# Optimization experiments

Measured on AMD Instinct MI355X. Metric: run time of the kernel, lower is better.

Reference implementation:

```python
import jax, jax.numpy as jnp
import numpy as np

N_NODES = 50000
N_EDGES = 600000
HIDDEN = 128
N_GRAPHS = 64


def _lin_params(key, din, dout):
    kw, kb = jax.random.split(key)
    W = jax.random.normal(kw, (din, dout), jnp.float32) / np.sqrt(din).astype(np.float32)
    b = jax.random.normal(kb, (dout,), jnp.float32) * 0.01
    return W, b


def setup_inputs() -> dict:
    key = jax.random.key(0)
    ks = jax.random.split(key, 12)
    node_weight = jax.random.uniform(ks[0], (N_NODES,), jnp.float32)
    edge_weight = jax.random.uniform(ks[1], (N_EDGES,), jnp.float32)
    edge_index = jax.random.randint(ks[2], (2, N_EDGES), 0, N_NODES, dtype=jnp.int64)
    batch = jnp.sort(jax.random.randint(ks[3], (N_NODES,), 0, N_GRAPHS, dtype=jnp.int64))
    Wn, bn = _lin_params(ks[4], 1, HIDDEN)
    We, be = _lin_params(ks[5], 1, HIDDEN)
    W1a, b1a = _lin_params(ks[6], HIDDEN, HIDDEN)
    W1b, b1b = _lin_params(ks[7], HIDDEN, HIDDEN)
    W2a, b2a = _lin_params(ks[8], HIDDEN, HIDDEN)
    W2b, b2b = _lin_params(ks[9], HIDDEN, HIDDEN)
    Wm1, bm1 = _lin_params(ks[10], HIDDEN, HIDDEN)
    Wm2, bm2 = _lin_params(ks[11], HIDDEN, 1)
    return dict(node_weight=node_weight, edge_weight=edge_weight, edge_index=edge_index,
                batch=batch, Wn=Wn, bn=bn, We=We, be=be,
                W1a=W1a, b1a=b1a, W1b=W1b, b1b=b1b,
                W2a=W2a, b2a=b2a, W2b=W2b, b2b=b2b,
                Wm1=Wm1, bm1=bm1, Wm2=Wm2, bm2=bm2)


def _gine(x, src, dst, edge_attr, Wa, ba, Wb, bb):
    # GINEConv (eps=0): h_i = nn( x_i + sum_{j->i} ReLU(x_j + e_ji) )
    msg = jax.nn.relu(x[src] + edge_attr)              # [E, H]
    agg = jax.ops.segment_sum(msg, dst, num_segments=N_NODES)  # [N, H]
    h = x + agg
    h = jax.nn.leaky_relu(h @ Wa + ba, 0.01)
    return h @ Wb + bb


def reference(node_weight, edge_weight, edge_index, batch,
              Wn, bn, We, be, W1a, b1a, W1b, b1b,
              W2a, b2a, W2b, b2b, Wm1, bm1, Wm2, bm2):
    src, dst = edge_index[0], edge_index[1]
    x = node_weight[:, None] @ Wn + bn                 # [N, H]
    e = edge_weight[:, None] @ We + be                 # [E, H]
    x = jax.nn.relu(_gine(x, src, dst, e, W1a, b1a, W1b, b1b))
    x = jax.nn.relu(_gine(x, src, dst, e, W2a, b2a, W2b, b2b))
    # global mean pool over graphs
    sums = jax.ops.segment_sum(x, batch, num_segments=N_GRAPHS)        # [G, H]
    cnts = jax.ops.segment_sum(jnp.ones((N_NODES,), x.dtype), batch, num_segments=N_GRAPHS)
    pooled = sums / jnp.maximum(cnts, 1.0)[:, None]
    h = jax.nn.leaky_relu(pooled @ Wm1 + bm1, 0.01)
    out = jax.nn.sigmoid(h @ Wm2 + bm2)                # [G, 1]
    return out[:, 0]
```

## Files before the change

### kernel.cpp

```cpp
#include <hip/hip_runtime.h>
#include <math.h>

#define NN 50000
#define NE 600000
#define HID 128
#define NG 64
#define CAP 48
#define ASTRH 136
#define NBIN 196
#define CHUNK 2344
#define TR 64

using half8v = __attribute__((ext_vector_type(8))) _Float16;
using half4v = __attribute__((ext_vector_type(4))) _Float16;
using half2v = __attribute__((ext_vector_type(2))) _Float16;
using f32x4  = __attribute__((ext_vector_type(4))) float;

__device__ __forceinline__ float unpack_w(unsigned p) {
  return (float)__builtin_bit_cast(_Float16, (unsigned short)(p & 0xffffu));
}

__global__ void k_prep(const int* __restrict__ batch, float* __restrict__ gsum,
                       int* __restrict__ pos,
                       const float* __restrict__ W1a, const float* __restrict__ W1b,
                       const float* __restrict__ W2a, const float* __restrict__ W2b,
                       _Float16* __restrict__ whi,
                       const int* __restrict__ dst, int* __restrict__ hist) {
  __shared__ int lh[NBIN];
  int b = blockIdx.x, t = threadIdx.x;
  if (b < 196) {
    int i = b * 256 + t;
    if (i < NN) {
      int bb = batch[i];
      if (i == 0) {
        for (int g = 0; g <= bb; ++g) pos[g] = 0;
      } else {
        int bp = batch[i - 1];
        for (int g = bp + 1; g <= bb; ++g) pos[g] = i;
      }
      if (i == NN - 1) {
        for (int g = bb + 1; g <= NG; ++g) pos[g] = NN;
      }
    }
  } else if (b < 204) {
    int i = (b - 196) * 256 + t;
    if (i < 2048) reinterpret_cast<float4*>(gsum)[i] = make_float4(0.f, 0.f, 0.f, 0.f);
  } else if (b < 236) {
    int tid = (b - 204) * 256 + t;
    int m = tid >> 11;
    const float* W = (m == 0) ? W1a : (m == 1) ? W1b : (m == 2) ? W2a : W2b;
    int rem = tid & 2047;
    int kt = rem >> 9;
    int fj = (rem >> 6) & 7;
    int l = rem & 63;
    int col = fj * 16 + (l & 15);
    int kbase = kt * 32 + (l >> 4) * 8;
    size_t obase = (size_t)m * 16384 + (size_t)(((kt * 8 + fj) * 64 + l)) * 8;
#pragma unroll
    for (int j = 0; j < 8; ++j) {
      whi[obase + j] = (_Float16)W[(size_t)(kbase + j) * HID + col];
    }
  } else {
    int hb = b - 236;
    if (t < NBIN) lh[t] = 0;
    __syncthreads();
    int lo = hb * CHUNK, hi = min(lo + CHUNK, NE);
    for (int e = lo + t; e < hi; e += 256) atomicAdd(&lh[dst[e] >> 8], 1);
    __syncthreads();
    if (t < NBIN) hist[t * 256 + hb] = lh[t];
  }
}

__global__ void k_scatter(const int* __restrict__ src, const int* __restrict__ dst,
                          const float* __restrict__ ew, const int* __restrict__ hist,
                          int* __restrict__ gbinbase, int2* __restrict__ part) {
  __shared__ int ps[256];
  __shared__ int cur[NBIN];
  int b = blockIdx.x, t = threadIdx.x;
  int sum0 = 0, T = 0;
  if (t < NBIN) {
    const int* row = &hist[t * 256];
#pragma unroll 4
    for (int i = 0; i < 256; ++i) {
      int v = row[i];
      T += v;
      sum0 += (i < b) ? v : 0;
    }
  }
  ps[t] = T;
  __syncthreads();
  for (int d = 1; d < 256; d <<= 1) {
    int u = (t >= d) ? ps[t - d] : 0;
    __syncthreads();
    ps[t] += u;
    __syncthreads();
  }
  if (t < NBIN) {
    int ebase = ps[t] - T;
    cur[t] = ebase + sum0;
    if (b == 0) gbinbase[t] = ebase;
  }
  if (b == 0 && t == 0) gbinbase[NBIN] = NE;
  __syncthreads();
  int lo = b * CHUNK, hi = min(lo + CHUNK, NE);
  for (int e = lo + t; e < hi; e += 256) {
    int d0 = dst[e];
    int p = atomicAdd(&cur[d0 >> 8], 1);
    _Float16 w = (_Float16)ew[e];
    unsigned wb = (unsigned)__builtin_bit_cast(unsigned short, w);
    part[p] = make_int2(src[e], ((d0 & 255) << 16) | (int)wb);
  }
}

__global__ void k_binfill(const int2* __restrict__ part, const int* __restrict__ gbinbase,
                          unsigned* __restrict__ bkt, int* __restrict__ deg) {
  __shared__ int cur[256];
  int j = blockIdx.x, t = threadIdx.x;
  cur[t] = 0;
  __syncthreads();
  int lo = gbinbase[j], hi = gbinbase[j + 1];
  for (int e = lo + t; e < hi; e += 256) {
    int2 q = part[e];
    int dl = q.y >> 16;
    int p = atomicAdd(&cur[dl], 1);
    if (p < CAP)
      bkt[(size_t)((j << 8) + dl) * CAP + p] =
          ((unsigned)q.x << 16) | ((unsigned)q.y & 0xffffu);
  }
  __syncthreads();
  int node = (j << 8) + t;
  if (node < NN) deg[node] = cur[t];
}

__global__ void k_layer1(const float* __restrict__ nw, const unsigned* __restrict__ bkt,
                         const int* __restrict__ deg,
                         const float* __restrict__ Wn, const float* __restrict__ bn,
                         const float* __restrict__ We, const float* __restrict__ be,
                         _Float16* __restrict__ h) {
  int wave = threadIdx.x >> 6;
  int lane = threadIdx.x & 63;
  int node = blockIdx.x * 4 + wave;
  if (node >= NN) return;
  int c = lane * 2;
  float wn0 = Wn[c], wn1 = Wn[c + 1];
  float we0 = We[c], we1 = We[c + 1];
  float bn0 = bn[c], bn1 = bn[c + 1];
  float cb0 = bn0 + be[c], cb1 = bn1 + be[c + 1];
  float ai = nw[node];
  float acc0 = fmaf(ai, wn0, bn0);
  float acc1 = fmaf(ai, wn1, bn1);
  int k0 = node * CAP;
  int cnt = min(deg[node], CAP);
  int k = 0;
  for (; k + 4 <= cnt; k += 4) {
    uint4 q = *reinterpret_cast<const uint4*>(&bkt[k0 + k]);
    float a0 = nw[q.x >> 16], a1 = nw[q.y >> 16];
    float a2 = nw[q.z >> 16], a3 = nw[q.w >> 16];
    float e0 = unpack_w(q.x), e1 = unpack_w(q.y);
    float e2 = unpack_w(q.z), e3 = unpack_w(q.w);
    acc0 += fmaxf(fmaf(a0, wn0, fmaf(e0, we0, cb0)), 0.f);
    acc1 += fmaxf(fmaf(a0, wn1, fmaf(e0, we1, cb1)), 0.f);
    acc0 += fmaxf(fmaf(a1, wn0, fmaf(e1, we0, cb0)), 0.f);
    acc1 += fmaxf(fmaf(a1, wn1, fmaf(e1, we1, cb1)), 0.f);
    acc0 += fmaxf(fmaf(a2, wn0, fmaf(e2, we0, cb0)), 0.f);
    acc1 += fmaxf(fmaf(a2, wn1, fmaf(e2, we1, cb1)), 0.f);
    acc0 += fmaxf(fmaf(a3, wn0, fmaf(e3, we0, cb0)), 0.f);
    acc1 += fmaxf(fmaf(a3, wn1, fmaf(e3, we1, cb1)), 0.f);
  }
  for (; k < cnt; ++k) {
    unsigned p = bkt[k0 + k];
    float a = nw[p >> 16];
    float b = unpack_w(p);
    acc0 += fmaxf(fmaf(a, wn0, fmaf(b, we0, cb0)), 0.f);
    acc1 += fmaxf(fmaf(a, wn1, fmaf(b, we1, cb1)), 0.f);
  }
  half2v o; o[0] = (_Float16)acc0; o[1] = (_Float16)acc1;
  *reinterpret_cast<half2v*>(&h[(size_t)node * HID + c]) = o;
}

__global__ void k_layer2(const _Float16* __restrict__ x1, const unsigned* __restrict__ bkt,
                         const int* __restrict__ deg,
                         const float* __restrict__ We, const float* __restrict__ be,
                         _Float16* __restrict__ h) {
  int wave = threadIdx.x >> 6;
  int l = threadIdx.x & 63;
  int half = l >> 5;
  int lane32 = l & 31;
  int node = blockIdx.x * 8 + wave * 2 + half;
  int c = lane32 * 4;
  float4 w4 = *reinterpret_cast<const float4*>(&We[c]);
  float4 b4 = *reinterpret_cast<const float4*>(&be[c]);
  half4v xs = *reinterpret_cast<const half4v*>(&x1[(size_t)node * HID + c]);
  float acc0 = (float)xs[0], acc1 = (float)xs[1];
  float acc2 = (float)xs[2], acc3 = (float)xs[3];
  int cnt = min(deg[node], CAP);
  int cntO = __shfl_xor(cnt, 32);
  int kmax = max(cnt, cntO);
  int k0 = node * CAP;

  for (int k = 0; k < kmax; k += 8) {
    uint4 qa = *reinterpret_cast<const uint4*>(&bkt[k0 + k]);
    uint4 qb = *reinterpret_cast<const uint4*>(&bkt[k0 + k + 4]);
    unsigned qs[8] = {qa.x, qa.y, qa.z, qa.w, qb.x, qb.y, qb.z, qb.w};
    half4v r[8];
#pragma unroll
    for (int i = 0; i < 8; ++i) {
      int s = min((int)(qs[i] >> 16), NN - 1);
      r[i] = *reinterpret_cast<const half4v*>(&x1[(size_t)s * HID + c]);
    }
#pragma unroll
    for (int i = 0; i < 8; ++i) {
      bool v = (k + i) < cnt;
      float e = unpack_w(qs[i]);
      float m0 = fmaxf((float)r[i][0] + fmaf(e, w4.x, b4.x), 0.f);
      float m1 = fmaxf((float)r[i][1] + fmaf(e, w4.y, b4.y), 0.f);
      float m2 = fmaxf((float)r[i][2] + fmaf(e, w4.z, b4.z), 0.f);
      float m3 = fmaxf((float)r[i][3] + fmaf(e, w4.w, b4.w), 0.f);
      acc0 += v ? m0 : 0.f;
      acc1 += v ? m1 : 0.f;
      acc2 += v ? m2 : 0.f;
      acc3 += v ? m3 : 0.f;
    }
  }
  half4v o;
  o[0] = (_Float16)acc0; o[1] = (_Float16)acc1;
  o[2] = (_Float16)acc2; o[3] = (_Float16)acc3;
  *reinterpret_cast<half4v*>(&h[(size_t)node * HID + c]) = o;
}

template <int POOL>
__global__ __launch_bounds__(256, 6) void k_mlp(
    const _Float16* __restrict__ X,
    const _Float16* __restrict__ Wah, const float* __restrict__ ba,
    const _Float16* __restrict__ Wbh, const float* __restrict__ bb,
    _Float16* __restrict__ Y,
    const int* __restrict__ batch, float* __restrict__ gsum) {
  extern __shared__ char smem_raw[];
  _Float16* Ah = (_Float16*)smem_raw;
  int* sB = (int*)(smem_raw + TR * ASTRH * 2);
  const int tid = threadIdx.x;
  const int l = tid & 63;
  const int wrow = (tid >> 6) * 16;
  const int rowBase = blockIdx.x * TR;

  if (POOL && tid < TR) sB[tid] = batch[min(rowBase + tid, NN - 1)];

  {
    int rr = tid >> 4;
    int c0 = (tid & 15) * 8;
#pragma unroll
    for (int p = 0; p < 4; ++p) {
      int r = p * 16 + rr;
      int srcRow = min(rowBase + r, NN - 1);
      half8v v = *reinterpret_cast<const half8v*>(&X[(size_t)srcRow * HID + c0]);
      *reinterpret_cast<half8v*>(&Ah[r * ASTRH + c0]) = v;
    }
  }
  __syncthreads();

  const int arow0 = wrow + (l & 15);
  const int kgrp = (l >> 4) * 8;
  const int lcol = l & 15;

  f32x4 acc[8];
#pragma unroll
  for (int j = 0; j < 8; ++j) acc[j] = f32x4{0.f, 0.f, 0.f, 0.f};

#pragma unroll
  for (int ks = 0; ks < 4; ++ks) {
    half8v a0 = *reinterpret_cast<const half8v*>(&Ah[arow0 * ASTRH + ks * 32 + kgrp]);
    const _Float16* wbh = &Wah[(size_t)((ks * 8) * 64 + l) * 8];
#pragma unroll
    for (int fj = 0; fj < 8; ++fj) {
      half8v bh = *reinterpret_cast<const half8v*>(wbh + fj * 512);
      acc[fj] = __builtin_amdgcn_mfma_f32_16x16x32_f16(a0, bh, acc[fj], 0, 0, 0);
    }
  }

  {
    float bal[8];
#pragma unroll
    for (int fj = 0; fj < 8; ++fj) bal[fj] = ba[fj * 16 + lcol];
    int rbase = wrow + ((l >> 4) << 2);
#pragma unroll
    for (int fj = 0; fj < 8; ++fj) {
#pragma unroll
      for (int r = 0; r < 4; ++r) {
        float v = acc[fj][r] + bal[fj];
        v = (v > 0.f) ? v : 0.01f * v;
        Ah[(rbase + r) * ASTRH + fj * 16 + lcol] = (_Float16)v;
      }
    }
  }

  f32x4 acc2[8];
#pragma unroll
  for (int j = 0; j < 8; ++j) acc2[j] = f32x4{0.f, 0.f, 0.f, 0.f};

#pragma unroll
  for (int ks = 0; ks < 4; ++ks) {
    half8v a0 = *reinterpret_cast<const half8v*>(&Ah[arow0 * ASTRH + ks * 32 + kgrp]);
    const _Float16* wbh = &Wbh[(size_t)((ks * 8) * 64 + l) * 8];
#pragma unroll
    for (int fj = 0; fj < 8; ++fj) {
      half8v bh = *reinterpret_cast<const half8v*>(wbh + fj * 512);
      acc2[fj] = __builtin_amdgcn_mfma_f32_16x16x32_f16(a0, bh, acc2[fj], 0, 0, 0);
    }
  }

  float bbl[8];
#pragma unroll
  for (int fj = 0; fj < 8; ++fj) bbl[fj] = bb[fj * 16 + lcol];
  const int rbase = wrow + ((l >> 4) << 2);

  if (!POOL) {
#pragma unroll
    for (int fj = 0; fj < 8; ++fj) {
#pragma unroll
      for (int r = 0; r < 4; ++r) {
        int row = rowBase + rbase + r;
        if (row < NN)
          Y[(size_t)row * HID + fj * 16 + lcol] =
              (_Float16)fmaxf(acc2[fj][r] + bbl[fj], 0.f);
      }
    }
  } else {
    __syncthreads();
    _Float16* sPh = (_Float16*)smem_raw;
#pragma unroll
    for (int fj = 0; fj < 8; ++fj) {
#pragma unroll
      for (int r = 0; r < 4; ++r) {
        bool ok = (rowBase + rbase + r) < NN;
        float z = fmaxf(acc2[fj][r] + bbl[fj], 0.f);
        sPh[(rbase + r) * 132 + fj * 16 + lcol] = (_Float16)(ok ? z : 0.f);
      }
    }
    __syncthreads();
    if (tid < HID) {
      int cur = sB[0];
      float run = 0.f;
      for (int r = 0; r < TR; ++r) {
        int g = sB[r];
        if (g != cur) {
          atomicAdd(&gsum[cur * HID + tid], run);
          run = 0.f; cur = g;
        }
        run += (float)sPh[r * 132 + tid];
      }
      atomicAdd(&gsum[cur * HID + tid], run);
    }
  }
}

__global__ void k_final(const float* __restrict__ gsum, const int* __restrict__ pos,
                        const float* __restrict__ Wm1, const float* __restrict__ bm1,
                        const float* __restrict__ Wm2, const float* __restrict__ bm2,
                        float* __restrict__ out) {
  __shared__ float sp[HID];
  __shared__ float red[HID];
  int g = blockIdx.x;
  int k = threadIdx.x;
  float c = fmaxf((float)(pos[g + 1] - pos[g]), 1.f);
  sp[k] = gsum[g * HID + k] / c;
  __syncthreads();
  float dot = 0.f;
  for (int j = 0; j < HID; ++j) dot = fmaf(sp[j], Wm1[j * HID + k], dot);
  float z = dot + bm1[k];
  z = (z > 0.f) ? z : 0.01f * z;
  red[k] = z * Wm2[k];
  __syncthreads();
  for (int s = 64; s > 0; s >>= 1) {
    if (k < s) red[k] += red[k + s];
    __syncthreads();
  }
  if (k == 0) out[g] = 1.f / (1.f + expf(-(red[0] + bm2[0])));
}

extern "C" void kernel_launch(void* const* d_in, const int* in_sizes, int n_in,
                              void* d_out, int out_size, void* d_ws, size_t ws_size,
                              hipStream_t stream) {
  const float* nw = (const float*)d_in[0];
  const float* ew = (const float*)d_in[1];
  const int* ei = (const int*)d_in[2];
  const int* src = ei;
  const int* dst = ei + NE;
  const int* batch = (const int*)d_in[3];
  const float* Wn = (const float*)d_in[4];
  const float* bn = (const float*)d_in[5];
  const float* We = (const float*)d_in[6];
  const float* be = (const float*)d_in[7];
  const float* W1a = (const float*)d_in[8];
  const float* b1a = (const float*)d_in[9];
  const float* W1b = (const float*)d_in[10];
  const float* b1b = (const float*)d_in[11];
  const float* W2a = (const float*)d_in[12];
  const float* b2a = (const float*)d_in[13];
  const float* W2b = (const float*)d_in[14];
  const float* b2b = (const float*)d_in[15];
  const float* Wm1 = (const float*)d_in[16];
  const float* bm1 = (const float*)d_in[17];
  const float* Wm2 = (const float*)d_in[18];
  const float* bm2 = (const float*)d_in[19];
  float* out = (float*)d_out;

  char* ws = (char*)d_ws;
  size_t o = 0;
  auto alloc = [&](size_t b) {
    size_t p = o;
    o += (b + 255) & ~(size_t)255;
    return p;
  };
  size_t deg_o = alloc(NN * 4);
  size_t gsum_o = alloc((size_t)NG * HID * 4);
  size_t pos_o = alloc((NG + 1) * 4);
  size_t hist_o = alloc((size_t)NBIN * 256 * 4);
  size_t gbb_o = alloc((NBIN + 1) * 4);
  size_t part_o = alloc((size_t)NE * 8);
  size_t bkt_o = alloc((size_t)NN * CAP * 4);
  size_t h1_o = alloc((size_t)NN * HID * 2);
  size_t x1_o = alloc((size_t)NN * HID * 2);
  size_t h2_o = alloc((size_t)NN * HID * 2);
  size_t whi_o = alloc((size_t)4 * 16384 * 2);

  int* deg = (int*)(ws + deg_o);
  float* gsum = (float*)(ws + gsum_o);
  int* pos = (int*)(ws + pos_o);
  int* hist = (int*)(ws + hist_o);
  int* gbinbase = (int*)(ws + gbb_o);
  int2* part = (int2*)(ws + part_o);
  unsigned* bkt = (unsigned*)(ws + bkt_o);
  _Float16* h1 = (_Float16*)(ws + h1_o);
  _Float16* x1h = (_Float16*)(ws + x1_o);
  _Float16* h2 = (_Float16*)(ws + h2_o);
  _Float16* whi = (_Float16*)(ws + whi_o);

  k_prep<<<492, 256, 0, stream>>>(batch, gsum, pos, W1a, W1b, W2a, W2b, whi,
                                  dst, hist);
  k_scatter<<<256, 256, 0, stream>>>(src, dst, ew, hist, gbinbase, part);
  k_binfill<<<NBIN, 256, 0, stream>>>(part, gbinbase, bkt, deg);

  k_layer1<<<NN / 4, 256, 0, stream>>>(nw, bkt, deg, Wn, bn, We, be, h1);

  size_t smem = (size_t)TR * ASTRH * 2 + TR * 4;
  const int mlpBlocks = (NN + TR - 1) / TR;
  k_mlp<0><<<mlpBlocks, 256, smem, stream>>>(h1, whi, b1a, whi + 16384, b1b,
                                             x1h, nullptr, nullptr);

  k_layer2<<<NN / 8, 256, 0, stream>>>(x1h, bkt, deg, We, be, h2);

  k_mlp<1><<<mlpBlocks, 256, smem, stream>>>(h2, whi + 2 * 16384, b2a,
                                             whi + 3 * 16384, b2b,
                                             nullptr, batch, gsum);

  k_final<<<NG, HID, 0, stream>>>(gsum, pos, Wm1, bm1, Wm2, bm2, out);
}
```

Measured before the change: 132.0 us.

## Merge CSR build kernels into cooperative kernel and fold final MLP into pool kernel

The three CSR-building kernels (prep, scatter, binfill) become one cooperative launch of 492 blocks, with grid-wide syncs between phases. The final graph-level MLP moves into the last block of the pooling MLP kernel, chosen with an atomic ticket. Together these remove three kernel launches and their inter-kernel gaps. In exchange, most blocks sit idle in the later phases of the cooperative kernel, grid.sync has its own cost, and the final MLP now runs serially in a single block.

After: 355.8 us. +169.6%, slower.

```diff
diff --git a/kernel.cpp b/kernel.cpp
--- a/kernel.cpp
+++ b/kernel.cpp
@@ -1,5 +1,8 @@
 #include <hip/hip_runtime.h>
+#include <hip/hip_cooperative_groups.h>
 #include <math.h>
+
+namespace cg = cooperative_groups;
 
 #define NN 50000
 #define NE 600000
@@ -10,6 +13,7 @@
 #define NBIN 196
 #define CHUNK 2344
 #define TR 64
+#define CSRG 492
 
 using half8v = __attribute__((ext_vector_type(8))) _Float16;
 using half4v = __attribute__((ext_vector_type(4))) _Float16;
@@ -20,14 +24,21 @@
   return (float)__builtin_bit_cast(_Float16, (unsigned short)(p & 0xffffu));
 }
 
-__global__ void k_prep(const int* __restrict__ batch, float* __restrict__ gsum,
-                       int* __restrict__ pos,
-                       const float* __restrict__ W1a, const float* __restrict__ W1b,
-                       const float* __restrict__ W2a, const float* __restrict__ W2b,
-                       _Float16* __restrict__ whi,
-                       const int* __restrict__ dst, int* __restrict__ hist) {
+__global__ void k_csr(const int* __restrict__ batch, float* __restrict__ gsum,
+                      int* __restrict__ pos, int* __restrict__ ticket,
+                      const float* __restrict__ W1a, const float* __restrict__ W1b,
+                      const float* __restrict__ W2a, const float* __restrict__ W2b,
+                      _Float16* __restrict__ whi,
+                      const int* __restrict__ src, const int* __restrict__ dst,
+                      const float* __restrict__ ew, int* __restrict__ hist,
+                      int* __restrict__ gbinbase, int2* __restrict__ part,
+                      unsigned* __restrict__ bkt, int* __restrict__ deg) {
+  cg::grid_group grid = cg::this_grid();
   __shared__ int lh[NBIN];
+  __shared__ int ps[256];
+  __shared__ int cur[256];
   int b = blockIdx.x, t = threadIdx.x;
+
   if (b < 196) {
     int i = b * 256 + t;
     if (i < NN) {
@@ -45,6 +56,7 @@
   } else if (b < 204) {
     int i = (b - 196) * 256 + t;
     if (i < 2048) reinterpret_cast<float4*>(gsum)[i] = make_float4(0.f, 0.f, 0.f, 0.f);
+    if (b == 196 && t == 0) *ticket = 0;
   } else if (b < 236) {
     int tid = (b - 204) * 256 + t;
     int m = tid >> 11;
@@ -69,67 +81,62 @@
     __syncthreads();
     if (t < NBIN) hist[t * 256 + hb] = lh[t];
   }
-}
-
-__global__ void k_scatter(const int* __restrict__ src, const int* __restrict__ dst,
-                          const float* __restrict__ ew, const int* __restrict__ hist,
-                          int* __restrict__ gbinbase, int2* __restrict__ part) {
-  __shared__ int ps[256];
-  __shared__ int cur[NBIN];
-  int b = blockIdx.x, t = threadIdx.x;
-  int sum0 = 0, T = 0;
-  if (t < NBIN) {
-    const int* row = &hist[t * 256];
+  grid.sync();
+
+  if (b >= 236) {
+    int hb = b - 236;
+    int sum0 = 0, T = 0;
+    if (t < NBIN) {
+      const int* row = &hist[t * 256];
 #pragma unroll 4
-    for (int i = 0; i < 256; ++i) {
-      int v = row[i];
-      T += v;
-      sum0 += (i < b) ? v : 0;
-    }
-  }
-  ps[t] = T;
-  __syncthreads();
-  for (int d = 1; d < 256; d <<= 1) {
-    int u = (t >= d) ? ps[t - d] : 0;
-    __syncthreads();
-    ps[t] += u;
-    __syncthreads();
-  }
-  if (t < NBIN) {
-    int ebase = ps[t] - T;
-    cur[t] = ebase + sum0;
-    if (b == 0) gbinbase[t] = ebase;
-  }
-  if (b == 0 && t == 0) gbinbase[NBIN] = NE;
-  __syncthreads();
-  int lo = b * CHUNK, hi = min(lo + CHUNK, NE);
-  for (int e = lo + t; e < hi; e += 256) {
-    int d0 = dst[e];
-    int p = atomicAdd(&cur[d0 >> 8], 1);
-    _Float16 w = (_Float16)ew[e];
-    unsigned wb = (unsigned)__builtin_bit_cast(unsigned short, w);
-    part[p] = make_int2(src[e], ((d0 & 255) << 16) | (int)wb);
-  }
-}
-
-__global__ void k_binfill(const int2* __restrict__ part, const int* __restrict__ gbinbase,
-                          unsigned* __restrict__ bkt, int* __restrict__ deg) {
-  __shared__ int cur[256];
-  int j = blockIdx.x, t = threadIdx.x;
-  cur[t] = 0;
-  __syncthreads();
-  int lo = gbinbase[j], hi = gbinbase[j + 1];
-  for (int e = lo + t; e < hi; e += 256) {
-    int2 q = part[e];
-    int dl = q.y >> 16;
-    int p = atomicAdd(&cur[dl], 1);
-    if (p < CAP)
-      bkt[(size_t)((j << 8) + dl) * CAP + p] =
-          ((unsigned)q.x << 16) | ((unsigned)q.y & 0xffffu);
-  }
-  __syncthreads();
-  int node = (j << 8) + t;
-  if (node < NN) deg[node] = cur[t];
+      for (int i = 0; i < 256; ++i) {
+        int v = row[i];
+        T += v;
+        sum0 += (i < hb) ? v : 0;
+      }
+    }
+    ps[t] = T;
+    __syncthreads();
+    for (int d = 1; d < 256; d <<= 1) {
+      int u = (t >= d) ? ps[t - d] : 0;
+      __syncthreads();
+      ps[t] += u;
+      __syncthreads();
+    }
+    if (t < NBIN) {
+      int ebase = ps[t] - T;
+      cur[t] = ebase + sum0;
+      if (hb == 0) gbinbase[t] = ebase;
+    }
+    if (hb == 0 && t == 0) gbinbase[NBIN] = NE;
+    __syncthreads();
+    int lo = hb * CHUNK, hi = min(lo + CHUNK, NE);
+    for (int e = lo + t; e < hi; e += 256) {
+      int d0 = dst[e];
+      int p = atomicAdd(&cur[d0 >> 8], 1);
+      _Float16 w = (_Float16)ew[e];
+      unsigned wb = (unsigned)__builtin_bit_cast(unsigned short, w);
+      part[p] = make_int2(src[e], ((d0 & 255) << 16) | (int)wb);
+    }
+  }
+  grid.sync();
+
+  if (b < NBIN) {
+    cur[t] = 0;
+    __syncthreads();
+    int lo = gbinbase[b], hi = gbinbase[b + 1];
+    for (int e = lo + t; e < hi; e += 256) {
+      int2 q = part[e];
+      int dl = q.y >> 16;
+      int p = atomicAdd(&cur[dl], 1);
+      if (p < CAP)
+        bkt[(size_t)((b << 8) + dl) * CAP + p] =
+            ((unsigned)q.x << 16) | ((unsigned)q.y & 0xffffu);
+    }
+    __syncthreads();
+    int node = (b << 8) + t;
+    if (node < NN) deg[node] = cur[t];
+  }
 }
 
 __global__ void k_layer1(const float* __restrict__ nw, const unsigned* __restrict__ bkt,
@@ -234,7 +241,11 @@
     const _Float16* __restrict__ Wah, const float* __restrict__ ba,
     const _Float16* __restrict__ Wbh, const float* __restrict__ bb,
     _Float16* __restrict__ Y,
-    const int* __restrict__ batch, float* __restrict__ gsum) {
+    const int* __restrict__ batch, float* __restrict__ gsum,
+    int* __restrict__ ticket, const int* __restrict__ pos,
+    const float* __restrict__ Wm1, const float* __restrict__ bm1,
+    const float* __restrict__ Wm2, const float* __restrict__ bm2,
+    float* __restrict__ out) {
   extern __shared__ char smem_raw[];
   _Float16* Ah = (_Float16*)smem_raw;
   int* sB = (int*)(smem_raw + TR * ASTRH * 2);
@@ -350,31 +361,42 @@
       }
       atomicAdd(&gsum[cur * HID + tid], run);
     }
-  }
-}
-
-__global__ void k_final(const float* __restrict__ gsum, const int* __restrict__ pos,
-                        const float* __restrict__ Wm1, const float* __restrict__ bm1,
-                        const float* __restrict__ Wm2, const float* __restrict__ bm2,
-                        float* __restrict__ out) {
-  __shared__ float sp[HID];
-  __shared__ float red[HID];
-  int g = blockIdx.x;
-  int k = threadIdx.x;
-  float c = fmaxf((float)(pos[g + 1] - pos[g]), 1.f);
-  sp[k] = gsum[g * HID + k] / c;
-  __syncthreads();
-  float dot = 0.f;
-  for (int j = 0; j < HID; ++j) dot = fmaf(sp[j], Wm1[j * HID + k], dot);
-  float z = dot + bm1[k];
-  z = (z > 0.f) ? z : 0.01f * z;
-  red[k] = z * Wm2[k];
-  __syncthreads();
-  for (int s = 64; s > 0; s >>= 1) {
-    if (k < s) red[k] += red[k + s];
-    __syncthreads();
-  }
-  if (k == 0) out[g] = 1.f / (1.f + expf(-(red[0] + bm2[0])));
+    __syncthreads();
+
+    __shared__ int isLast;
+    __shared__ float invc[NG];
+    __shared__ float red2[NG];
+    if (tid == 0) {
+      __threadfence();
+      int tk = atomicAdd(ticket, 1);
+      isLast = (tk == (int)gridDim.x - 1);
+    }
+    __syncthreads();
+    if (!isLast) return;
+    __threadfence();
+    if (tid < NG) {
+      invc[tid] = 1.f / fmaxf((float)(pos[tid + 1] - pos[tid]), 1.f);
+      red2[tid] = 0.f;
+    }
+    __syncthreads();
+    int kk = tid & 127;
+    int gp = tid >> 7;
+    float wm2k = Wm2[kk];
+    for (int i = 0; i < 32; ++i) {
+      int g = 2 * i + gp;
+      float dot = 0.f;
+      for (int j = 0; j < HID; ++j)
+        dot = fmaf(gsum[g * HID + j], Wm1[j * HID + kk], dot);
+      float z = fmaf(dot, invc[g], bm1[kk]);
+      z = (z > 0.f) ? z : 0.01f * z;
+      float v = z * wm2k;
+#pragma unroll
+      for (int off = 32; off; off >>= 1) v += __shfl_xor(v, off);
+      if ((tid & 63) == 0) atomicAdd(&red2[g], v);
+    }
+    __syncthreads();
+    if (tid < NG) out[tid] = 1.f / (1.f + expf(-(red2[tid] + bm2[0])));
+  }
 }
 
 extern "C" void kernel_launch(void* const* d_in, const int* in_sizes, int n_in,
@@ -383,8 +405,8 @@
   const float* nw = (const float*)d_in[0];
   const float* ew = (const float*)d_in[1];
   const int* ei = (const int*)d_in[2];
-  const int* src = ei;
-  const int* dst = ei + NE;
+  const int* srcp = ei;
+  const int* dstp = ei + NE;
   const int* batch = (const int*)d_in[3];
   const float* Wn = (const float*)d_in[4];
   const float* bn = (const float*)d_in[5];
@@ -414,6 +436,7 @@
   size_t deg_o = alloc(NN * 4);
   size_t gsum_o = alloc((size_t)NG * HID * 4);
   size_t pos_o = alloc((NG + 1) * 4);
+  size_t tick_o = alloc(256);
   size_t hist_o = alloc((size_t)NBIN * 256 * 4);
   size_t gbb_o = alloc((NBIN + 1) * 4);
   size_t part_o = alloc((size_t)NE * 8);
@@ -426,6 +449,7 @@
   int* deg = (int*)(ws + deg_o);
   float* gsum = (float*)(ws + gsum_o);
   int* pos = (int*)(ws + pos_o);
+  int* ticket = (int*)(ws + tick_o);
   int* hist = (int*)(ws + hist_o);
   int* gbinbase = (int*)(ws + gbb_o);
   int2* part = (int2*)(ws + part_o);
@@ -435,23 +459,29 @@
   _Float16* h2 = (_Float16*)(ws + h2_o);
   _Float16* whi = (_Float16*)(ws + whi_o);
 
-  k_prep<<<492, 256, 0, stream>>>(batch, gsum, pos, W1a, W1b, W2a, W2b, whi,
-                                  dst, hist);
-  k_scatter<<<256, 256, 0, stream>>>(src, dst, ew, hist, gbinbase, part);
-  k_binfill<<<NBIN, 256, 0, stream>>>(part, gbinbase, bkt, deg);
+  {
+    void* args[] = {(void*)&batch, (void*)&gsum, (void*)&pos, (void*)&ticket,
+                    (void*)&W1a, (void*)&W1b, (void*)&W2a, (void*)&W2b,
+                    (void*)&whi, (void*)&srcp, (void*)&dstp, (void*)&ew,
+                    (void*)&hist, (void*)&gbinbase, (void*)&part,
+                    (void*)&bkt, (void*)&deg};
+    hipLaunchCooperativeKernel(reinterpret_cast<const void*>(&k_csr),
+                               dim3(CSRG), dim3(256), args, 0, stream);
+  }
 
   k_layer1<<<NN / 4, 256, 0, stream>>>(nw, bkt, deg, Wn, bn, We, be, h1);
 
   size_t smem = (size_t)TR * ASTRH * 2 + TR * 4;
   const int mlpBlocks = (NN + TR - 1) / TR;
   k_mlp<0><<<mlpBlocks, 256, smem, stream>>>(h1, whi, b1a, whi + 16384, b1b,
-                                             x1h, nullptr, nullptr);
+                                             x1h, nullptr, nullptr, nullptr,
+                                             nullptr, nullptr, nullptr, nullptr,
+                                             nullptr, nullptr);
 
   k_layer2<<<NN / 8, 256, 0, stream>>>(x1h, bkt, deg, We, be, h2);
 
   k_mlp<1><<<mlpBlocks, 256, smem, stream>>>(h2, whi + 2 * 16384, b2a,
                                              whi + 3 * 16384, b2b,
-                                             nullptr, batch, gsum);
-
-  k_final<<<NG, HID, 0, stream>>>(gsum, pos, Wm1, bm1, Wm2, bm2, out);
-}
+                                             nullptr, batch, gsum,
+                                             ticket, pos, Wm1, bm1, Wm2, bm2, out);
+}
```
